# Performance work log

Hardware: AMD Instinct MI355X
Metric: run time of the kernel (lower is better)

Reference implementation:

```python
import jax, jax.numpy as jnp
import numpy as np

H = 125      # LSTM hidden per direction
MLP = 100    # hidden_MLP
N = 1024     # sentence length


def _lstm_dir(x, wih, whh, bih, bhh, reverse):
    # x: [n, din]; torch gate order i, f, g, o
    b = bih + bhh
    def step(carry, xt):
        h, c = carry
        g = xt @ wih.T + h @ whh.T + b
        i, f, gg, o = jnp.split(g, 4)
        c = jax.nn.sigmoid(f) * c + jax.nn.sigmoid(i) * jnp.tanh(gg)
        h = jax.nn.sigmoid(o) * jnp.tanh(c)
        return (h, c), h
    z = jnp.zeros((H,), x.dtype)
    _, hs = jax.lax.scan(step, (z, z), x, reverse=reverse)
    return hs  # [n, H]


def _bilstm(x, pf, pb):
    return jnp.concatenate([_lstm_dir(x, *pf, reverse=False),
                            _lstm_dir(x, *pb, reverse=True)], axis=-1)


def setup_inputs() -> dict:
    key = jax.random.key(0)
    ks = iter(jax.random.split(key, 32))
    p = lambda shape, s=0.1: jax.random.normal(next(ks), shape, jnp.float32) * s
    inp = {}
    inp["word_idx"] = jax.random.randint(next(ks), (1, N), 0, 15948)
    inp["pos_idx"] = jax.random.randint(next(ks), (1, N), 0, 47)
    inp["true_tree_heads"] = jax.random.randint(next(ks), (N,), 0, N)
    inp["word_emb"] = p((15948, 100), 1.0)
    inp["pos_emb"] = p((47, 25), 1.0)
    for l, din in ((0, 125), (1, 250)):
        for d in ("f", "b"):
            inp[f"w_ih_{l}{d}"] = p((4 * H, din))
            inp[f"w_hh_{l}{d}"] = p((4 * H, H))
            inp[f"b_ih_{l}{d}"] = p((4 * H,))
            inp[f"b_hh_{l}{d}"] = p((4 * H,))
    inp["w1"] = p((MLP, 2 * H)); inp["b1"] = p((MLP,))
    inp["w2"] = p((MLP, 2 * H)); inp["b2"] = p((MLP,))
    inp["w3"] = p((MLP,)); inp["b3"] = p(())
    return inp


def reference(word_idx, pos_idx, true_tree_heads, word_emb, pos_emb,
              w_ih_0f, w_hh_0f, b_ih_0f, b_hh_0f,
              w_ih_0b, w_hh_0b, b_ih_0b, b_hh_0b,
              w_ih_1f, w_hh_1f, b_ih_1f, b_hh_1f,
              w_ih_1b, w_hh_1b, b_ih_1b, b_hh_1b,
              w1, b1, w2, b2, w3, b3):
    # embeddings: [n, 125]
    emb = jnp.concatenate([word_emb[word_idx[0]], pos_emb[pos_idx[0]]], axis=-1)
    h0 = _bilstm(emb, (w_ih_0f, w_hh_0f, b_ih_0f, b_hh_0f),
                 (w_ih_0b, w_hh_0b, b_ih_0b, b_hh_0b))            # [n, 250]
    h1 = _bilstm(h0, (w_ih_1f, w_hh_1f, b_ih_1f, b_hh_1f),
                 (w_ih_1b, w_hh_1b, b_ih_1b, b_hh_1b))            # [n, 250]
    heads = h1 @ w1.T + b1   # [n, 100]
    mods = h1 @ w2.T + b2    # [n, 100]
    # tag_scores[h, m] = layer3(tanh(heads[h] + mods[m])), diagonal = -inf
    s = jnp.tanh(heads[:, None, :] + mods[None, :, :])            # [n, n, 100]
    scores = jnp.einsum('hmd,d->hm', s, w3) + b3
    n = scores.shape[0]
    return jnp.where(jnp.eye(n, dtype=bool), -jnp.inf, scores)
```

## Files before the change

kernel.cpp:

```cpp
#include <hip/hip_runtime.h>
#include <hip/hip_bf16.h>

#define H 125
#define G4 500
#define NN 1024
#define DMLP 100

#define SCL1 (-1.4426950408889634f)
#define SCL2 (-2.8853900817779268f)

typedef __attribute__((ext_vector_type(4))) float f32x4;
typedef __attribute__((ext_vector_type(4))) int   i32x4;
typedef __attribute__((ext_vector_type(8))) int   i32x8;

__device__ __forceinline__ float frcp(float x) { return __builtin_amdgcn_rcpf(x); }
__device__ __forceinline__ float fexp2(float x) {
    float r;
    asm("v_exp_f32 %0, %1" : "=v"(r) : "v"(x));
    return r;
}

__device__ __forceinline__ float bf16_quant(float v) {
    return __bfloat162float(__float2bfloat16(v));
}

__global__ __launch_bounds__(512) void ingemm4a_k(
    const int* __restrict__ wid, const int* __restrict__ pid,
    const float* __restrict__ wemb, const float* __restrict__ pemb,
    const float* __restrict__ wf, const float* __restrict__ bif, const float* __restrict__ bhf,
    const float* __restrict__ wb, const float* __restrict__ bib, const float* __restrict__ bhb,
    float* __restrict__ xg4f, float* __restrict__ xg4b)
{
    __shared__ float xs[8][125];
    const int dir = blockIdx.y;
    const float* __restrict__ w  = dir ? wb  : wf;
    const float* __restrict__ bi = dir ? bib : bif;
    const float* __restrict__ bh = dir ? bhb : bhf;
    float* __restrict__ xg       = dir ? xg4b : xg4f;

    const int t0  = blockIdx.x * 8;
    const int tid = threadIdx.x;
    for (int i = tid; i < 8 * 125; i += 512) {
        int r = i / 125, k = i - r * 125;
        int t = t0 + r;
        xs[r][k] = (k < 100) ? wemb[wid[t] * 100 + k] : pemb[pid[t] * 25 + (k - 100)];
    }
    __syncthreads();

    if (tid < G4) {
        const int g = tid / 125;
        const int u = tid - g * 125;
        const float sg = (g == 2) ? SCL2 : SCL1;
        const float* wr = w + tid * 125;
        float base = bi[tid] + bh[tid];
        float acc[8];
#pragma unroll
        for (int tt = 0; tt < 8; ++tt) acc[tt] = base;
        for (int k = 0; k < 125; ++k) {
            float wv = wr[k];
#pragma unroll
            for (int tt = 0; tt < 8; ++tt) acc[tt] += wv * xs[tt][k];
        }
#pragma unroll
        for (int tt = 0; tt < 8; ++tt) xg[(t0 + tt) * 512 + u * 4 + g] = acc[tt] * sg;
    } else {
        const int qq = tid - G4;
#pragma unroll
        for (int tt = 0; tt < 8; ++tt) xg[(t0 + tt) * 512 + G4 + qq] = 0.f;
    }
}

__global__ __launch_bounds__(512) void ingemm4_k(
    const float* __restrict__ x,
    const float* __restrict__ wf, const float* __restrict__ bif, const float* __restrict__ bhf,
    const float* __restrict__ wb, const float* __restrict__ bib, const float* __restrict__ bhb,
    float* __restrict__ xg4f, float* __restrict__ xg4b)
{
    __shared__ float xs[8][250];
    const int dir = blockIdx.y;
    const float* __restrict__ w  = dir ? wb  : wf;
    const float* __restrict__ bi = dir ? bib : bif;
    const float* __restrict__ bh = dir ? bhb : bhf;
    float* __restrict__ xg       = dir ? xg4b : xg4f;

    const int t0  = blockIdx.x * 8;
    const int tid = threadIdx.x;
    for (int i = tid; i < 8 * 250; i += 512) {
        int r = i / 250;
        xs[r][i - r * 250] = x[t0 * 250 + i];
    }
    __syncthreads();

    if (tid < G4) {
        const int g = tid / 125;
        const int u = tid - g * 125;
        const float sg = (g == 2) ? SCL2 : SCL1;
        const float* wr = w + tid * 250;
        float base = bi[tid] + bh[tid];
        float acc[8];
#pragma unroll
        for (int tt = 0; tt < 8; ++tt) acc[tt] = base;
        for (int k = 0; k < 250; ++k) {
            float wv = wr[k];
#pragma unroll
            for (int tt = 0; tt < 8; ++tt) acc[tt] += wv * xs[tt][k];
        }
#pragma unroll
        for (int tt = 0; tt < 8; ++tt) xg[(t0 + tt) * 512 + u * 4 + g] = acc[tt] * sg;
    } else {
        const int qq = tid - G4;
#pragma unroll
        for (int tt = 0; tt < 8; ++tt) xg[(t0 + tt) * 512 + G4 + qq] = 0.f;
    }
}

__global__ __launch_bounds__(64) void whhprep8_k(
    const float* __restrict__ w0f, const float* __restrict__ w0b,
    const float* __restrict__ w1f, const float* __restrict__ w1b,
    int* __restrict__ out0, int* __restrict__ out1)
{
    const int lay = blockIdx.z;
    const int dir = blockIdx.y;
    const float* __restrict__ whh = lay ? (dir ? w1b : w1f) : (dir ? w0b : w0f);
    int* __restrict__ out = lay ? out1 : out0;
    const int tg = blockIdx.x;
    const int l  = threadIdx.x;
    const int R  = tg * 16 + (l & 15);
    const int u  = R >> 2, g = R & 3;
    const float sg = (g == 2) ? SCL2 : SCL1;
    const int kb = (l >> 4) * 32;
    float f[32];
#pragma unroll
    for (int e = 0; e < 32; ++e) {
        const int k = kb + e;
        f[e] = (u < H && k < H) ? whh[(g * H + u) * H + k] * sg : 0.f;
    }
    int* dst = out + ((dir * 32 + tg) * 64 + l) * 8;
#pragma unroll
    for (int j = 0; j < 8; ++j) {
        int lo = __builtin_amdgcn_cvt_pk_fp8_f32(f[4 * j + 0], f[4 * j + 1], 0,  false);
        int wv = __builtin_amdgcn_cvt_pk_fp8_f32(f[4 * j + 2], f[4 * j + 3], lo, true);
        dst[j] = wv;
    }
}

__global__ __launch_bounds__(512, 1) void lstm_scan10_k(
    const float* __restrict__ xg_f, const float* __restrict__ xg_b,
    const int* __restrict__ whhA,
    float* __restrict__ hout)
{
    __shared__ __align__(16) unsigned char hb8[128];
    __shared__ __align__(16) float gates[128 * 4];
    const int dir = blockIdx.x;
    const float* __restrict__ xg = dir ? xg_b : xg_f;
    const int col = dir ? H : 0;

    const int tid = threadIdx.x;
    const int w = tid >> 6;
    const int l = tid & 63;
    const int q = l >> 4;
    const int c = l & 15;

    const i32x8* Ab = (const i32x8*)whhA;
    i32x8 A0 = Ab[(dir * 32 + w * 4 + 0) * 64 + l];
    i32x8 A1 = Ab[(dir * 32 + w * 4 + 1) * 64 + l];
    i32x8 A2 = Ab[(dir * 32 + w * 4 + 2) * 64 + l];
    i32x8 A3 = Ab[(dir * 32 + w * 4 + 3) * 64 + l];

    if (tid < 128) hb8[tid] = 0;
    __syncthreads();
    if (tid < 128) __builtin_amdgcn_s_setprio(1);

    const int usel = 16 * w + 4 * (c & 3) + q;
    const bool writer = (c < 4);
    const int xoff = 4 * usel;

    float cst = 0.f;
    auto T = [&](int s) { return dir ? (NN - 1 - s) : s; };

    auto LOADX = [&](int s_) -> f32x4 {
        const int sc = (s_ < NN) ? s_ : NN - 1;
        return *(const f32x4*)(xg + T(sc) * 512 + xoff);
    };

    auto STEP = [&](int t, f32x4 x) {
        i32x8 B = *(const i32x8*)(hb8 + 32 * q);
        f32x4 a0 = __builtin_amdgcn_mfma_scale_f32_16x16x128_f8f6f4(
            A0, B, x, 0, 0, 0, 0x7F7F7F7F, 0, 0x7F7F7F7F);
        f32x4 a1 = __builtin_amdgcn_mfma_scale_f32_16x16x128_f8f6f4(
            A1, B, x, 0, 0, 0, 0x7F7F7F7F, 0, 0x7F7F7F7F);
        f32x4 a2 = __builtin_amdgcn_mfma_scale_f32_16x16x128_f8f6f4(
            A2, B, x, 0, 0, 0, 0x7F7F7F7F, 0, 0x7F7F7F7F);
        f32x4 a3 = __builtin_amdgcn_mfma_scale_f32_16x16x128_f8f6f4(
            A3, B, x, 0, 0, 0, 0x7F7F7F7F, 0, 0x7F7F7F7F);
        if (writer) {
            f32x4 s0 = (c & 1) ? a1 : a0;
            f32x4 s1 = (c & 1) ? a3 : a2;
            f32x4 gv = (c & 2) ? s1 : s0;
            *(f32x4*)(gates + 4 * usel) = gv;
        }
        asm volatile("s_waitcnt lgkmcnt(0)" ::: "memory");
        __builtin_amdgcn_s_barrier();
        __builtin_amdgcn_sched_barrier(0);
        if (tid < 128) {
            f32x4 g = *(const f32x4*)(gates + 4 * tid);
            const float ai = frcp(1.f + fexp2(g.x));
            const float af = frcp(1.f + fexp2(g.y));
            const float sgm = frcp(1.f + fexp2(g.z));
            const float ao = frcp(1.f + fexp2(g.w));
            const float ag = __builtin_fmaf(2.f, sgm, -1.f);
            cst = __builtin_fmaf(af, cst, ai * ag);
            const float r = frcp(1.f + fexp2(cst * SCL2));
            const float hv = __builtin_fmaf(2.f * ao, r, -ao);
            int pk = __builtin_amdgcn_cvt_pk_fp8_f32(hv, 0.f, 0, false);
            hb8[tid] = (unsigned char)(pk & 0xFF);
            if (tid < H) hout[t * 250 + col + tid] = hv;
        }
        asm volatile("s_waitcnt lgkmcnt(0)" ::: "memory");
        __builtin_amdgcn_s_barrier();
        __builtin_amdgcn_sched_barrier(0);
    };

    f32x4 p0 = LOADX(0), p1 = LOADX(1);
#pragma unroll 1
    for (int s = 0; s < NN; s += 4) {
        f32x4 n0 = LOADX(s + 2), n1 = LOADX(s + 3);
        STEP(T(s),     p0);
        STEP(T(s + 1), p1);
        p0 = LOADX(s + 4); p1 = LOADX(s + 5);
        STEP(T(s + 2), n0);
        STEP(T(s + 3), n1);
    }
}

__global__ __launch_bounds__(256) void headmod_k(
    const float* __restrict__ h1,
    const float* __restrict__ w1, const float* __restrict__ b1,
    const float* __restrict__ w2, const float* __restrict__ b2,
    float* __restrict__ heads, float* __restrict__ mods)
{
    __shared__ float xs[8][250];
    const int t0  = blockIdx.x * 8;
    const int tid = threadIdx.x;
    for (int i = tid; i < 8 * 250; i += 256) {
        int r = i / 250;
        xs[r][i - r * 250] = h1[t0 * 250 + i];
    }
    __syncthreads();

    int d; const float* w; float bb; float* o;
    if (tid < DMLP)                          { d = tid;       w = w1 + d * 250; bb = b1[d]; o = heads; }
    else if (tid >= 128 && tid < 128 + DMLP) { d = tid - 128; w = w2 + d * 250; bb = b2[d]; o = mods;  }
    else return;

    float acc[8];
#pragma unroll
    for (int tt = 0; tt < 8; ++tt) acc[tt] = bb;
    for (int k = 0; k < 250; ++k) {
        float wv = w[k];
#pragma unroll
        for (int tt = 0; tt < 8; ++tt) acc[tt] += wv * xs[tt][k];
    }
#pragma unroll
    for (int tt = 0; tt < 8; ++tt) o[(t0 + tt) * DMLP + d] = acc[tt];
}

__global__ __launch_bounds__(256) void scores_k(
    const float* __restrict__ heads, const float* __restrict__ mods,
    const float* __restrict__ w3, const float* __restrict__ b3,
    float* __restrict__ out)
{
    __shared__ __align__(16) float hh[16][DMLP];
    __shared__ __align__(16) float mm[16][DMLP];
    __shared__ __align__(16) float ws3[DMLP];
    const int bh = blockIdx.y * 16, bm = blockIdx.x * 16;
    const int tid = threadIdx.x;
    for (int i = tid; i < 16 * DMLP; i += 256) {
        int r = i / DMLP, d = i - r * DMLP;
        hh[r][d] = heads[(bh + r) * DMLP + d];
        mm[r][d] = mods[(bm + r) * DMLP + d];
    }
    if (tid < DMLP) ws3[tid] = w3[tid];
    __syncthreads();

    const int tx = tid & 15, ty = tid >> 4;
    const f32x4* h4 = (const f32x4*)hh[ty];
    const f32x4* m4 = (const f32x4*)mm[tx];
    const f32x4* w4 = (const f32x4*)ws3;
    float acc = 0.f;
#pragma unroll
    for (int qq = 0; qq < DMLP / 4; ++qq) {
        f32x4 v  = h4[qq] + m4[qq];
        f32x4 wv = w4[qq];
#pragma unroll
        for (int e = 0; e < 4; ++e) {
            float th = 2.f * frcp(1.f + fexp2(v[e] * SCL2)) - 1.f;
            acc += wv[e] * th;
        }
    }
    acc += b3[0];
    const int hrow = bh + ty, mcol = bm + tx;
    float v = (hrow == mcol) ? -3.3895313892515355e38f : bf16_quant(acc);
    out[hrow * NN + mcol] = v;
}

extern "C" void kernel_launch(void* const* d_in, const int* in_sizes, int n_in,
                              void* d_out, int out_size, void* d_ws, size_t ws_size,
                              hipStream_t stream)
{
    const int*   wid   = (const int*)d_in[0];
    const int*   pid   = (const int*)d_in[1];
    const float* wemb  = (const float*)d_in[3];
    const float* pemb  = (const float*)d_in[4];
    const float* wih0f = (const float*)d_in[5];
    const float* whh0f = (const float*)d_in[6];
    const float* bih0f = (const float*)d_in[7];
    const float* bhh0f = (const float*)d_in[8];
    const float* wih0b = (const float*)d_in[9];
    const float* whh0b = (const float*)d_in[10];
    const float* bih0b = (const float*)d_in[11];
    const float* bhh0b = (const float*)d_in[12];
    const float* wih1f = (const float*)d_in[13];
    const float* whh1f = (const float*)d_in[14];
    const float* bih1f = (const float*)d_in[15];
    const float* bhh1f = (const float*)d_in[16];
    const float* wih1b = (const float*)d_in[17];
    const float* whh1b = (const float*)d_in[18];
    const float* bih1b = (const float*)d_in[19];
    const float* bhh1b = (const float*)d_in[20];
    const float* w1    = (const float*)d_in[21];
    const float* b1    = (const float*)d_in[22];
    const float* w2    = (const float*)d_in[23];
    const float* b2    = (const float*)d_in[24];
    const float* w3    = (const float*)d_in[25];
    const float* b3    = (const float*)d_in[26];

    float* ws    = (float*)d_ws;
    float* xgf   = ws;
    float* xgb   = ws + 524288;
    float* h0    = ws + 1048576;
    float* h1    = ws + 1304576;
    float* hd    = ws + 1560576;
    float* md    = ws + 1662976;
    int*   whhA0 = (int*)(ws + 1765376);
    int*   whhA1 = (int*)(ws + 1798144);

    whhprep8_k<<<dim3(32, 2, 2), 64, 0, stream>>>(
        whh0f, whh0b, whh1f, whh1b, whhA0, whhA1);

    ingemm4a_k<<<dim3(NN / 8, 2), 512, 0, stream>>>(
        wid, pid, wemb, pemb,
        wih0f, bih0f, bhh0f, wih0b, bih0b, bhh0b, xgf, xgb);

    lstm_scan10_k<<<2, 512, 0, stream>>>(xgf, xgb, whhA0, h0);

    ingemm4_k<<<dim3(NN / 8, 2), 512, 0, stream>>>(
        h0, wih1f, bih1f, bhh1f, wih1b, bih1b, bhh1b, xgf, xgb);

    lstm_scan10_k<<<2, 512, 0, stream>>>(xgf, xgb, whhA1, h1);

    headmod_k<<<NN / 8, 256, 0, stream>>>(h1, w1, b1, w2, b2, hd, md);

    scores_k<<<dim3(NN / 16, NN / 16), 256, 0, stream>>>(hd, md, w3, b3, (float*)d_out);
}
```

Measured before the change: 1.004 ms.

## Fuse LSTM cell update into MFMA writer lanes with double-buffered hidden state

The writer lanes that hold each unit's four gate pre-activations now apply the cell nonlinearities directly in registers. Before, the gates went through shared memory to a separate 128-thread phase. The hidden-state byte buffer is double-buffered, so each time step needs one barrier instead of two, and the gate staging round trip through LDS is gone. The cell state now lives in the writer lanes, and the s_setprio hint has been removed.

```diff
diff --git a/kernel.cpp b/kernel.cpp
--- a/kernel.cpp
+++ b/kernel.cpp
@@ -144,13 +144,12 @@
     }
 }
 
-__global__ __launch_bounds__(512, 1) void lstm_scan10_k(
+__global__ __launch_bounds__(512, 1) void lstm_scan11_k(
     const float* __restrict__ xg_f, const float* __restrict__ xg_b,
     const int* __restrict__ whhA,
     float* __restrict__ hout)
 {
-    __shared__ __align__(16) unsigned char hb8[128];
-    __shared__ __align__(16) float gates[128 * 4];
+    __shared__ __align__(16) unsigned char hb8[2][128];
     const int dir = blockIdx.x;
     const float* __restrict__ xg = dir ? xg_b : xg_f;
     const int col = dir ? H : 0;
@@ -167,15 +166,15 @@
     i32x8 A2 = Ab[(dir * 32 + w * 4 + 2) * 64 + l];
     i32x8 A3 = Ab[(dir * 32 + w * 4 + 3) * 64 + l];
 
-    if (tid < 128) hb8[tid] = 0;
-    __syncthreads();
-    if (tid < 128) __builtin_amdgcn_s_setprio(1);
+    if (tid < 256) ((unsigned char*)hb8)[tid] = 0;
+    __syncthreads();
 
     const int usel = 16 * w + 4 * (c & 3) + q;
     const bool writer = (c < 4);
     const int xoff = 4 * usel;
 
     float cst = 0.f;
+    int pp = 0;
     auto T = [&](int s) { return dir ? (NN - 1 - s) : s; };
 
     auto LOADX = [&](int s_) -> f32x4 {
@@ -184,7 +183,7 @@
     };
 
     auto STEP = [&](int t, f32x4 x) {
-        i32x8 B = *(const i32x8*)(hb8 + 32 * q);
+        i32x8 B = *(const i32x8*)(hb8[pp] + 32 * q);
         f32x4 a0 = __builtin_amdgcn_mfma_scale_f32_16x16x128_f8f6f4(
             A0, B, x, 0, 0, 0, 0x7F7F7F7F, 0, 0x7F7F7F7F);
         f32x4 a1 = __builtin_amdgcn_mfma_scale_f32_16x16x128_f8f6f4(
@@ -193,32 +192,28 @@
             A2, B, x, 0, 0, 0, 0x7F7F7F7F, 0, 0x7F7F7F7F);
         f32x4 a3 = __builtin_amdgcn_mfma_scale_f32_16x16x128_f8f6f4(
             A3, B, x, 0, 0, 0, 0x7F7F7F7F, 0, 0x7F7F7F7F);
+
+        float hv = 0.f;
         if (writer) {
             f32x4 s0 = (c & 1) ? a1 : a0;
             f32x4 s1 = (c & 1) ? a3 : a2;
             f32x4 gv = (c & 2) ? s1 : s0;
-            *(f32x4*)(gates + 4 * usel) = gv;
+            const float ai  = frcp(1.f + fexp2(gv.x));
+            const float af  = frcp(1.f + fexp2(gv.y));
+            const float sgm = frcp(1.f + fexp2(gv.z));
+            const float ao  = frcp(1.f + fexp2(gv.w));
+            const float ag  = __builtin_fmaf(2.f, sgm, -1.f);
+            cst = __builtin_fmaf(af, cst, ai * ag);
+            const float r = frcp(1.f + fexp2(cst * SCL2));
+            hv = __builtin_fmaf(2.f * ao, r, -ao);
+            int pk = __builtin_amdgcn_cvt_pk_fp8_f32(hv, 0.f, 0, false);
+            hb8[pp ^ 1][usel] = (unsigned char)(pk & 0xFF);
         }
         asm volatile("s_waitcnt lgkmcnt(0)" ::: "memory");
         __builtin_amdgcn_s_barrier();
         __builtin_amdgcn_sched_barrier(0);
-        if (tid < 128) {
-            f32x4 g = *(const f32x4*)(gates + 4 * tid);
-            const float ai = frcp(1.f + fexp2(g.x));
-            const float af = frcp(1.f + fexp2(g.y));
-            const float sgm = frcp(1.f + fexp2(g.z));
-            const float ao = frcp(1.f + fexp2(g.w));
-            const float ag = __builtin_fmaf(2.f, sgm, -1.f);
-            cst = __builtin_fmaf(af, cst, ai * ag);
-            const float r = frcp(1.f + fexp2(cst * SCL2));
-            const float hv = __builtin_fmaf(2.f * ao, r, -ao);
-            int pk = __builtin_amdgcn_cvt_pk_fp8_f32(hv, 0.f, 0, false);
-            hb8[tid] = (unsigned char)(pk & 0xFF);
-            if (tid < H) hout[t * 250 + col + tid] = hv;
-        }
-        asm volatile("s_waitcnt lgkmcnt(0)" ::: "memory");
-        __builtin_amdgcn_s_barrier();
-        __builtin_amdgcn_sched_barrier(0);
+        if (writer && usel < H) hout[t * 250 + col + usel] = hv;
+        pp ^= 1;
     };
 
     f32x4 p0 = LOADX(0), p1 = LOADX(1);
@@ -352,12 +347,12 @@
         wid, pid, wemb, pemb,
         wih0f, bih0f, bhh0f, wih0b, bih0b, bhh0b, xgf, xgb);
 
-    lstm_scan10_k<<<2, 512, 0, stream>>>(xgf, xgb, whhA0, h0);
+    lstm_scan11_k<<<2, 512, 0, stream>>>(xgf, xgb, whhA0, h0);
 
     ingemm4_k<<<dim3(NN / 8, 2), 512, 0, stream>>>(
         h0, wih1f, bih1f, bhh1f, wih1b, bih1b, bhh1b, xgf, xgb);
 
-    lstm_scan10_k<<<2, 512, 0, stream>>>(xgf, xgb, whhA1, h1);
+    lstm_scan11_k<<<2, 512, 0, stream>>>(xgf, xgb, whhA1, h1);
 
     headmod_k<<<NN / 8, 256, 0, stream>>>(h1, w1, b1, w2, b2, hd, md);
 
```

Result: faster. 866.6 us (median of 2 runs) (-13.7%).
